# Performance work log

Measured on AMD Instinct MI355X. Metric: run time of the kernel, lower is better.

The kernel has to match this reference:

```python
import jax, jax.numpy as jnp
import numpy as np

B, D, ND, N2, H = 16384, 512, 4, 32, 4
C = D  # attention channels (per-detector feature dim)
EPS = 1e-5


def setup_inputs() -> dict:
    key = jax.random.key(0)
    ks = jax.random.split(key, 8)
    rn = lambda k, s, sc: jax.random.normal(k, s, jnp.float32) * sc
    return {
        'x': jax.random.normal(ks[0], (B, D), jnp.float32),
        'bn1_g': jnp.ones(D * ND, jnp.float32), 'bn1_b': jnp.zeros(D * ND, jnp.float32),
        'w1': rn(ks[1], (ND, D, D), 1e-4),  # diagonal blocks of the masked EnsembleLinear weight
        'bn2_g': jnp.ones(D * ND, jnp.float32), 'bn2_b': jnp.zeros(D * ND, jnp.float32),
        'wq': rn(ks[2], (C, D), 0.02), 'bq': jnp.zeros(C, jnp.float32),
        'wk': rn(ks[3], (C, D), 0.02), 'bk': jnp.zeros(C, jnp.float32),
        'wv': rn(ks[4], (C, D), 0.02), 'bv': jnp.zeros(C, jnp.float32),
        'wo': rn(ks[5], (C, C), 0.02), 'bo': jnp.zeros(C, jnp.float32),
        'ln1_g': jnp.ones(C, jnp.float32), 'ln1_b': jnp.zeros(C, jnp.float32),
        'wff': rn(ks[6], (C, C), 0.02), 'bff': jnp.zeros(C, jnp.float32),
        'ln2_g': jnp.ones(C, jnp.float32), 'ln2_b': jnp.zeros(C, jnp.float32),
        'w2': rn(ks[7], (ND, N2, D), 1e-4),
        'bn3_g': jnp.ones(N2 * ND, jnp.float32), 'bn3_b': jnp.zeros(N2 * ND, jnp.float32),
    }


def _batchnorm(x, g, b):
    # training-mode BatchNorm1d: biased batch stats over the batch axis
    m = x.mean(0)
    v = ((x - m) ** 2).mean(0)
    return (x - m) * jax.lax.rsqrt(v + EPS) * g + b


def _layernorm(x, g, b):
    m = x.mean(-1, keepdims=True)
    v = ((x - m) ** 2).mean(-1, keepdims=True)
    return (x - m) * jax.lax.rsqrt(v + EPS) * g + b


def reference(x, bn1_g, bn1_b, w1, bn2_g, bn2_b, wq, bq, wk, bk, wv, bv, wo, bo,
              ln1_g, ln1_b, wff, bff, ln2_g, ln2_b, w2, bn3_g, bn3_b):
    n = x.shape[0]
    # concat x num_detectors times along features: [n, ND*D]
    xc = jnp.tile(x, (1, ND))
    h = _batchnorm(xc, bn1_g, bn1_b)
    # EnsembleLinear 1: block-diagonal masked matmul == one small GEMM per detector
    h = jnp.einsum('ndi,doi->ndo', h.reshape(n, ND, D), w1).reshape(n, ND * D)
    h = jax.nn.sigmoid(_batchnorm(h, bn2_g, bn2_b))
    # 4-token self-attention over detectors: t is [n, ND, D]
    t = h.reshape(n, ND, D)
    hd = C // H
    q = (t @ wq.T + bq).reshape(n, ND, H, hd).transpose(0, 2, 1, 3)  # [n,H,S,hd]
    k = (t @ wk.T + bk).reshape(n, ND, H, hd).transpose(0, 2, 1, 3)
    v = (t @ wv.T + bv).reshape(n, ND, H, hd).transpose(0, 2, 1, 3)
    scale = jnp.sqrt(jnp.float32(C / H))
    scores = jnp.einsum('nhqd,nhkd->nhqk', q, k) / scale
    attn = jax.nn.softmax(scores, axis=-1)
    o = jnp.einsum('nhqk,nhkd->nhqd', attn, v).transpose(0, 2, 1, 3).reshape(n, ND, C)
    o = o @ wo.T + bo
    a1 = _layernorm(o + t, ln1_g, ln1_b)
    a2 = _layernorm(a1 @ wff.T + bff + a1, ln2_g, ln2_b)
    # EnsembleLinear 2: per-detector D -> N2
    h2 = jnp.einsum('ndi,doi->ndo', a2, w2).reshape(n, ND * N2)
    out = jax.nn.sigmoid(_batchnorm(h2, bn3_g, bn3_b))
    return out
```

## Files before the change

### kernel.cpp

```cpp
#include <hip/hip_runtime.h>
#include <hip/hip_bf16.h>

#define EPS 1e-5f

typedef __attribute__((ext_vector_type(8))) short bf16x8;
typedef __attribute__((ext_vector_type(4))) float f32x4;
typedef __attribute__((ext_vector_type(4))) float float4v;

__device__ __forceinline__ float b2f(short u) {
    union { unsigned int i; float f; } x;
    x.i = ((unsigned int)(unsigned short)u) << 16;
    return x.f;
}
__device__ __forceinline__ short f2b(float f) {
    unsigned int x = __builtin_bit_cast(unsigned int, f);
    unsigned int r = (x + 0x7FFFu + ((x >> 16) & 1u)) >> 16;
    return (short)r;
}

__device__ __forceinline__ void load_lds16(const void* g, void* l) {
    __builtin_amdgcn_global_load_lds(
        (const __attribute__((address_space(1))) unsigned int*)g,
        (__attribute__((address_space(3))) unsigned int*)l, 16, 0, 0);
}


__device__ __forceinline__ void cast8(const float* __restrict__ src, short* __restrict__ dst, long idx) {
    const float4v* s = (const float4v*)src;
    float4v a = s[idx * 2], b = s[idx * 2 + 1];
    bf16x8 o;
    o[0] = f2b(a[0]); o[1] = f2b(a[1]); o[2] = f2b(a[2]); o[3] = f2b(a[3]);
    o[4] = f2b(b[0]); o[5] = f2b(b[1]); o[6] = f2b(b[2]); o[7] = f2b(b[3]);
    *(bf16x8*)(dst + idx * 8) = o;
}

__global__ __launch_bounds__(256) void k_prep(
    const float* __restrict__ wq, const float* __restrict__ wk, const float* __restrict__ wv,
    const float* __restrict__ wo, const float* __restrict__ wff, const float* __restrict__ w2,
    const float* __restrict__ bq, const float* __restrict__ bk, const float* __restrict__ bv,
    short* __restrict__ Wqkvb, short* __restrict__ wo_b, short* __restrict__ wff_b,
    short* __restrict__ w2_b, float* __restrict__ bqkv) {
    int bid = blockIdx.x, tid = threadIdx.x;
    if (bid < 640) {
        int seg = bid >> 7;
        long idx = (long)(bid & 127) * 256 + tid;
        const float* src;
        short* dst;
        if (seg == 0) { src = wq; dst = Wqkvb; }
        else if (seg == 1) { src = wk; dst = Wqkvb + 262144; }
        else if (seg == 2) { src = wv; dst = Wqkvb + 524288; }
        else if (seg == 3) { src = wo; dst = wo_b; }
        else { src = wff; dst = wff_b; }
        cast8(src, dst, idx);
    } else if (bid < 672) {
        long idx = (long)(bid - 640) * 256 + tid;
        cast8(w2, w2_b, idx);
    } else {
        int i = (bid - 672) * 256 + tid;
        if (i < 512) bqkv[i] = bq[i];
        else if (i < 1024) bqkv[i] = bk[i - 512];
        else if (i < 1536) bqkv[i] = bv[i - 1024];
    }
}

__global__ __launch_bounds__(256) void k_statcast_x(const float* __restrict__ x,
                                                    short* __restrict__ xb,
                                                    float* __restrict__ psum, float* __restrict__ psq) {
    int b = blockIdx.x, tid = threadIdx.x;
    const float* xp = x + (long)b * 64 * 512;
    short* xo = xb + (long)b * 64 * 512;
    float s0 = 0, q0 = 0, s1 = 0, q1 = 0;
    for (int r = 0; r < 64; ++r) {
        float v0 = xp[r * 512 + tid];
        float v1 = xp[r * 512 + tid + 256];
        xo[r * 512 + tid] = f2b(v0);
        xo[r * 512 + tid + 256] = f2b(v1);
        s0 += v0; q0 += v0 * v0; s1 += v1; q1 += v1 * v1;
    }
    psum[b * 512 + tid] = s0; psum[b * 512 + tid + 256] = s1;
    psq[b * 512 + tid] = q0;  psq[b * 512 + tid + 256] = q1;
}


__global__ __launch_bounds__(256) void k_finalize_meanrs(const float* __restrict__ psum,
                                                         const float* __restrict__ psq,
                                                         int nparts, int ncols, float invB,
                                                         float* __restrict__ mean, float* __restrict__ rs) {
    int l = threadIdx.x & 63, grp = threadIdx.x >> 6;
    int c = blockIdx.x * 64 + l;
    float s = 0, q = 0;
    for (int p = grp; p < nparts; p += 4) {
        s += psum[(long)p * ncols + c];
        q += psq[(long)p * ncols + c];
    }
    __shared__ float rs_[4][64], rq_[4][64];
    rs_[grp][l] = s; rq_[grp][l] = q;
    __syncthreads();
    if (grp == 0) {
        s = rs_[0][l] + rs_[1][l] + rs_[2][l] + rs_[3][l];
        q = rq_[0][l] + rq_[1][l] + rq_[2][l] + rq_[3][l];
        float m = s * invB;
        float v = q * invB - m * m;
        mean[c] = m;
        rs[c] = rsqrtf(v + EPS);
    }
}

__global__ __launch_bounds__(256) void k_finalize_ss(const float* __restrict__ psum,
                                                     const float* __restrict__ psq,
                                                     int nparts, int ncols, float invB,
                                                     const float* __restrict__ g, const float* __restrict__ bb,
                                                     float* __restrict__ scale, float* __restrict__ shift) {
    int l = threadIdx.x & 63, grp = threadIdx.x >> 6;
    int c = blockIdx.x * 64 + l;
    float s = 0, q = 0;
    for (int p = grp; p < nparts; p += 4) {
        s += psum[(long)p * ncols + c];
        q += psq[(long)p * ncols + c];
    }
    __shared__ float rs_[4][64], rq_[4][64];
    rs_[grp][l] = s; rq_[grp][l] = q;
    __syncthreads();
    if (grp == 0) {
        s = rs_[0][l] + rs_[1][l] + rs_[2][l] + rs_[3][l];
        q = rq_[0][l] + rq_[1][l] + rq_[2][l] + rq_[3][l];
        float m = s * invB, v = q * invB - m * m;
        float sc = g[c] * rsqrtf(v + EPS);
        scale[c] = sc;
        shift[c] = bb[c] - m * sc;
    }
}

__global__ __launch_bounds__(256) void k_fold_w1(const float* __restrict__ w1, const float* __restrict__ g1,
                                                 const float* __restrict__ b1, const float* __restrict__ mean,
                                                 const float* __restrict__ rs,
                                                 short* __restrict__ W1b, float* __restrict__ beff) {
    int bx = blockIdx.x;
    int d = bx >> 9, tid = threadIdx.x;
    const float* wrow = w1 + (long)bx * 512;
    float part = 0.f;
    for (int i = tid; i < 512; i += 256) {
        float wv = wrow[i];
        float sc = rs[i] * g1[d * 512 + i];
        W1b[(long)bx * 512 + i] = f2b(wv * sc);
        part += (b1[d * 512 + i] - mean[i] * sc) * wv;
    }
    __shared__ float red[256];
    red[tid] = part;
    __syncthreads();
    for (int st = 128; st > 0; st >>= 1) {
        if (tid < st) red[tid] += red[tid + st];
        __syncthreads();
    }
    if (tid == 0) beff[bx] = red[0];
}

__global__ __launch_bounds__(256) void k_bnsig(const short* h, short* t,
                                               const float* __restrict__ scale,
                                               const float* __restrict__ shift) {
    long i8 = ((long)blockIdx.x * 256 + threadIdx.x) * 8;
    int c0 = (int)(i8 & 2047);
    bf16x8 v = *(const bf16x8*)(h + i8);
    bf16x8 o;
#pragma unroll
    for (int j = 0; j < 8; ++j) {
        float x = b2f(v[j]) * scale[c0 + j] + shift[c0 + j];
        o[j] = f2b(1.f / (1.f + __expf(-x)));
    }
    *(bf16x8*)(t + i8) = o;
}

__global__ __launch_bounds__(256) void k_ln(const short* in, short* out,
                                            const float* __restrict__ g, const float* __restrict__ bb) {
    int w = threadIdx.x >> 6, lane = threadIdx.x & 63;
    long row = (long)blockIdx.x * 4 + w;
    const short* rp = in + row * 512;
    bf16x8 v = *(const bf16x8*)(rp + lane * 8);
    float f[8];
    float s = 0.f;
#pragma unroll
    for (int j = 0; j < 8; ++j) { f[j] = b2f(v[j]); s += f[j]; }
#pragma unroll
    for (int m = 1; m < 64; m <<= 1) s += __shfl_xor(s, m, 64);
    float mean = s * (1.f / 512.f);
    float q = 0.f;
#pragma unroll
    for (int j = 0; j < 8; ++j) { float d = f[j] - mean; q += d * d; }
#pragma unroll
    for (int m = 1; m < 64; m <<= 1) q += __shfl_xor(q, m, 64);
    float rs = rsqrtf(q * (1.f / 512.f) + EPS);
    bf16x8 o;
#pragma unroll
    for (int j = 0; j < 8; ++j) {
        int c = lane * 8 + j;
        o[j] = f2b((f[j] - mean) * rs * g[c] + bb[c]);
    }
    *(bf16x8*)(out + row * 512 + lane * 8) = o;
}

__global__ __launch_bounds__(256) void k_bn3sig(const float* __restrict__ pre, float* __restrict__ out,
                                                const float* __restrict__ scale, const float* __restrict__ shift) {
    long i4 = ((long)blockIdx.x * 256 + threadIdx.x) * 4;
    float4v v = *(const float4v*)(pre + i4);
    int c0 = (int)(i4 & 127);
    float4v o;
#pragma unroll
    for (int j = 0; j < 4; ++j) {
        float x = v[j] * scale[c0 + j] + shift[c0 + j];
        o[j] = 1.f / (1.f + __expf(-x));
    }
    *(float4v*)(out + i4) = o;
}


template <int BM, int BN, int WGM, int WGN, bool ADD_RES, bool OUT_BF16>
__global__ __launch_bounds__(WGM* WGN * 64) void k_gemm_bt(
    const short* __restrict__ A, int a_zoff, int lda,
    const short* __restrict__ W, int w_zoff,
    const float* __restrict__ bias, int bias_zoff,
    short* Cb, float* Cf, int c_zoff, int ldc,
    const short* R, int ldr, int K) {
    constexpr int BK = 32;
    constexpr int WM = BM / WGM, WN = BN / WGN;
    constexpr int AM = WM / 16, AN = WN / 16;
    constexpr int NT = WGM * WGN * 64;
    constexpr int CH = (BM + BN) * (BK / 8);
    constexpr bool DBUF = (CH % NT == 0) && (CH / NT == 4);

    int tid = threadIdx.x;
    int wave = tid >> 6, lane = tid & 63;
    int wm = (wave % WGM) * WM, wn = (wave / WGM) * WN;

    int bm_idx = blockIdx.x, bn_idx = blockIdx.y;
    if (gridDim.z == 1 && (gridDim.x & 7) == 0) {
        int flat = blockIdx.x + gridDim.x * blockIdx.y;
        int k = flat & 7, l = flat >> 3;
        int j = l / gridDim.y;
        bn_idx = l - j * gridDim.y;
        bm_idx = k + 8 * j;
    }
    long m0 = (long)bm_idx * BM;
    int n0 = bn_idx * BN;
    int z = blockIdx.z;
    const short* Az = A + (long)z * a_zoff;
    const short* Wz = W + (long)z * w_zoff;

    f32x4 acc[AM][AN];
#pragma unroll
    for (int i = 0; i < AM; ++i)
#pragma unroll
        for (int j = 0; j < AN; ++j)
#pragma unroll
            for (int q = 0; q < 4; ++q) acc[i][j][q] = 0.f;

    int fr = lane & 15, ko = (lane >> 4) * 8;
    int cr = (lane >> 4) * 4, cc = lane & 15;

    if constexpr (DBUF) {
        __shared__ alignas(16) short Smem[2][(BM + BN) * BK];
        auto stage = [&](int b, int k0) {
#pragma unroll
            for (int i = 0; i < 4; ++i) {
                int c = tid + i * NT;
                int row = c >> 2, koff = (c & 3) * 8;
                const short* g = (row < BM) ? (Az + (m0 + row) * lda + k0 + koff)
                                            : (Wz + (long)(n0 + row - BM) * K + k0 + koff);
                load_lds16(g, (char*)Smem[b] + (size_t)c * 16);
            }
        };
        stage(0, 0);
        int nk = K / BK;
        for (int kt = 0; kt < nk; ++kt) {
            int b = kt & 1;
            if (kt + 1 < nk) {
                stage(b ^ 1, (kt + 1) * BK);
                asm volatile("s_waitcnt vmcnt(4)" ::: "memory");
            } else {
                asm volatile("s_waitcnt vmcnt(0)" ::: "memory");
            }
            __builtin_amdgcn_s_barrier();
            bf16x8 af[AM], bfr[AN];
#pragma unroll
            for (int i = 0; i < AM; ++i)
                af[i] = *(const bf16x8*)(&Smem[b][(wm + i * 16 + fr) * BK + ko]);
#pragma unroll
            for (int j = 0; j < AN; ++j)
                bfr[j] = *(const bf16x8*)(&Smem[b][(BM + wn + j * 16 + fr) * BK + ko]);
#pragma unroll
            for (int i = 0; i < AM; ++i)
#pragma unroll
                for (int j = 0; j < AN; ++j)
                    acc[i][j] = __builtin_amdgcn_mfma_f32_16x16x32_bf16(af[i], bfr[j], acc[i][j], 0, 0, 0);
            asm volatile("s_waitcnt lgkmcnt(0)" ::: "memory");
            __builtin_amdgcn_s_barrier();
        }
    } else {
        __shared__ alignas(16) short Smem[(BM + BN) * BK];
        for (int k0 = 0; k0 < K; k0 += BK) {
#pragma unroll
            for (int c = tid; c < CH; c += NT) {
                int row = c >> 2, koff = (c & 3) * 8;
                const short* g = (row < BM) ? (Az + (m0 + row) * lda + k0 + koff)
                                            : (Wz + (long)(n0 + row - BM) * K + k0 + koff);
                load_lds16(g, (char*)Smem + (size_t)c * 16);
            }
            __syncthreads();
            bf16x8 af[AM], bfr[AN];
#pragma unroll
            for (int i = 0; i < AM; ++i) af[i] = *(const bf16x8*)(&Smem[(wm + i * 16 + fr) * BK + ko]);
#pragma unroll
            for (int j = 0; j < AN; ++j) bfr[j] = *(const bf16x8*)(&Smem[(BM + wn + j * 16 + fr) * BK + ko]);
#pragma unroll
            for (int i = 0; i < AM; ++i)
#pragma unroll
                for (int j = 0; j < AN; ++j)
                    acc[i][j] = __builtin_amdgcn_mfma_f32_16x16x32_bf16(af[i], bfr[j], acc[i][j], 0, 0, 0);
            __syncthreads();
        }
    }

#pragma unroll
    for (int i = 0; i < AM; ++i) {
#pragma unroll
        for (int j = 0; j < AN; ++j) {
            int col = n0 + wn + j * 16 + cc;
            float bv = bias ? bias[(long)z * bias_zoff + col] : 0.f;
#pragma unroll
            for (int q = 0; q < 4; ++q) {
                long row = m0 + wm + i * 16 + cr + q;
                float v = acc[i][j][q] + bv;
                if constexpr (ADD_RES) v += b2f(R[row * (long)ldr + col]);
                long idx = row * (long)ldc + (long)z * c_zoff + col;
                if constexpr (OUT_BF16) Cb[idx] = f2b(v);
                else Cf[idx] = v;
            }
        }
    }
}


__global__ __launch_bounds__(256) void k_gemm_e1(
    const short* __restrict__ A, const short* __restrict__ W1, const float* __restrict__ beff,
    short* __restrict__ h, float* __restrict__ psum, float* __restrict__ psq) {
    constexpr int BK = 32;
    __shared__ alignas(16) short Smem[2][256 * BK];
    __shared__ float cS[2][128], cQ[2][128];

    int tid = threadIdx.x;
    int wave = tid >> 6, lane = tid & 63;
    int wm = (wave & 1) * 64, wn = (wave >> 1) * 64;
    long m0 = (long)blockIdx.x * 128;
    int n0 = blockIdx.y * 128;
    int z = blockIdx.z;
    const short* Wz = W1 + (long)z * 512 * 512;

    f32x4 acc[4][4];
#pragma unroll
    for (int i = 0; i < 4; ++i)
#pragma unroll
        for (int j = 0; j < 4; ++j)
#pragma unroll
            for (int q = 0; q < 4; ++q) acc[i][j][q] = 0.f;

    int fr = lane & 15, ko = (lane >> 4) * 8;

    auto stage = [&](int b, int k0) {
#pragma unroll
        for (int i = 0; i < 4; ++i) {
            int c = tid + i * 256;
            int row = c >> 2, koff = (c & 3) * 8;
            const short* g = (row < 128) ? (A + (m0 + row) * 512 + k0 + koff)
                                         : (Wz + (long)(n0 + row - 128) * 512 + k0 + koff);
            load_lds16(g, (char*)Smem[b] + (size_t)c * 16);
        }
    };
    stage(0, 0);
    for (int kt = 0; kt < 16; ++kt) {
        int b = kt & 1;
        if (kt + 1 < 16) {
            stage(b ^ 1, (kt + 1) * BK);
            asm volatile("s_waitcnt vmcnt(4)" ::: "memory");
        } else {
            asm volatile("s_waitcnt vmcnt(0)" ::: "memory");
        }
        __builtin_amdgcn_s_barrier();
        bf16x8 af[4], bfr[4];
#pragma unroll
        for (int i = 0; i < 4; ++i) af[i] = *(const bf16x8*)(&Smem[b][(wm + i * 16 + fr) * BK + ko]);
#pragma unroll
        for (int j = 0; j < 4; ++j) bfr[j] = *(const bf16x8*)(&Smem[b][(128 + wn + j * 16 + fr) * BK + ko]);
#pragma unroll
        for (int i = 0; i < 4; ++i)
#pragma unroll
            for (int j = 0; j < 4; ++j)
                acc[i][j] = __builtin_amdgcn_mfma_f32_16x16x32_bf16(af[i], bfr[j], acc[i][j], 0, 0, 0);
        asm volatile("s_waitcnt lgkmcnt(0)" ::: "memory");
        __builtin_amdgcn_s_barrier();
    }

    int cr = (lane >> 4) * 4, cc = lane & 15;
    float bv[4], colS[4], colQ[4];
#pragma unroll
    for (int j = 0; j < 4; ++j) {
        bv[j] = beff[z * 512 + n0 + wn + j * 16 + cc];
        colS[j] = 0.f; colQ[j] = 0.f;
    }
#pragma unroll
    for (int i = 0; i < 4; ++i)
#pragma unroll
        for (int j = 0; j < 4; ++j)
#pragma unroll
            for (int q = 0; q < 4; ++q) {
                float v = acc[i][j][q] + bv[j];
                acc[i][j][q] = v;
                colS[j] += v; colQ[j] += v * v;
            }
#pragma unroll
    for (int i = 0; i < 4; ++i)
#pragma unroll
        for (int q = 0; q < 4; ++q) {
            long row = m0 + wm + i * 16 + cr + q;
            short* hp = h + row * 2048 + z * 512 + n0 + wn + cc;
#pragma unroll
            for (int j = 0; j < 4; ++j) hp[j * 16] = f2b(acc[i][j][q]);
        }
#pragma unroll
    for (int j = 0; j < 4; ++j) {
        float s = colS[j], qq = colQ[j];
        s += __shfl_xor(s, 16, 64); s += __shfl_xor(s, 32, 64);
        qq += __shfl_xor(qq, 16, 64); qq += __shfl_xor(qq, 32, 64);
        if (lane < 16) { cS[wave & 1][wn + j * 16 + cc] = s; cQ[wave & 1][wn + j * 16 + cc] = qq; }
    }
    __syncthreads();
    if (tid < 128) {
        float S = cS[0][tid] + cS[1][tid];
        float Q = cQ[0][tid] + cQ[1][tid];
        psum[(long)blockIdx.x * 2048 + z * 512 + n0 + tid] = S;
        psq[(long)blockIdx.x * 2048 + z * 512 + n0 + tid] = Q;
    }
}


__global__ __launch_bounds__(256) void k_gemm_e2(
    const short* __restrict__ A, int a_zoff, int lda,
    const short* __restrict__ W2,
    float* __restrict__ Cf, int ldc,
    float* __restrict__ psum, float* __restrict__ psq) {
    constexpr int BK = 32;
    __shared__ alignas(16) short Smem[(128 + 32) * BK];
    __shared__ float cS[4][32], cQ[4][32];

    int tid = threadIdx.x;
    int wave = tid >> 6, lane = tid & 63;
    int wm = wave * 32;
    long m0 = (long)blockIdx.x * 128;
    int z = blockIdx.z;
    const short* Az = A + (long)z * a_zoff;
    const short* Wz = W2 + (long)z * 32 * 512;

    f32x4 acc[2][2];
#pragma unroll
    for (int i = 0; i < 2; ++i)
#pragma unroll
        for (int j = 0; j < 2; ++j)
#pragma unroll
            for (int q = 0; q < 4; ++q) acc[i][j][q] = 0.f;

    int fr = lane & 15, ko = (lane >> 4) * 8;

    for (int k0 = 0; k0 < 512; k0 += BK) {
        for (int c = tid; c < 640; c += 256) {
            int row = c >> 2, koff = (c & 3) * 8;
            const short* g = (row < 128) ? (Az + (m0 + row) * lda + k0 + koff)
                                         : (Wz + (long)(row - 128) * 512 + k0 + koff);
            load_lds16(g, (char*)Smem + (size_t)c * 16);
        }
        __syncthreads();
        bf16x8 af[2], bfr[2];
#pragma unroll
        for (int i = 0; i < 2; ++i) af[i] = *(const bf16x8*)(&Smem[(wm + i * 16 + fr) * BK + ko]);
#pragma unroll
        for (int j = 0; j < 2; ++j) bfr[j] = *(const bf16x8*)(&Smem[(128 + j * 16 + fr) * BK + ko]);
#pragma unroll
        for (int i = 0; i < 2; ++i)
#pragma unroll
            for (int j = 0; j < 2; ++j)
                acc[i][j] = __builtin_amdgcn_mfma_f32_16x16x32_bf16(af[i], bfr[j], acc[i][j], 0, 0, 0);
        __syncthreads();
    }

    int cr = (lane >> 4) * 4, cc = lane & 15;
    float colS[2] = {0.f, 0.f}, colQ[2] = {0.f, 0.f};
#pragma unroll
    for (int i = 0; i < 2; ++i)
#pragma unroll
        for (int q = 0; q < 4; ++q) {
            long row = m0 + wm + i * 16 + cr + q;
            float* cp = Cf + row * (long)ldc + z * 32 + cc;
#pragma unroll
            for (int j = 0; j < 2; ++j) {
                float v = acc[i][j][q];
                cp[j * 16] = v;
                colS[j] += v; colQ[j] += v * v;
            }
        }
#pragma unroll
    for (int j = 0; j < 2; ++j) {
        float s = colS[j], qq = colQ[j];
        s += __shfl_xor(s, 16, 64); s += __shfl_xor(s, 32, 64);
        qq += __shfl_xor(qq, 16, 64); qq += __shfl_xor(qq, 32, 64);
        if (lane < 16) { cS[wave][j * 16 + cc] = s; cQ[wave][j * 16 + cc] = qq; }
    }
    __syncthreads();
    if (tid < 32) {
        float S = cS[0][tid] + cS[1][tid] + cS[2][tid] + cS[3][tid];
        float Q = cQ[0][tid] + cQ[1][tid] + cQ[2][tid] + cQ[3][tid];
        psum[(long)blockIdx.x * 128 + z * 32 + tid] = S;
        psq[(long)blockIdx.x * 128 + z * 32 + tid] = Q;
    }
}

__global__ __launch_bounds__(256) void k_attn(const short* __restrict__ qkv, short* __restrict__ ao) {
    __shared__ alignas(16) short lds[4][4][1544];
    __shared__ float attn_s[4][4][4][4];
    int w = threadIdx.x >> 6, lane = threadIdx.x & 63;
    long n = (long)blockIdx.x * 4 + w;
    const short* src = qkv + n * 4 * 1536;
#pragma unroll
    for (int c = 0; c < 12; ++c) {
        int e = c * 512 + lane * 8;
        *(bf16x8*)(&lds[w][e / 1536][e % 1536]) = *(const bf16x8*)(src + e);
    }
    __syncthreads();
    int h = lane >> 4, a = (lane >> 2) & 3, b = lane & 3;
    const short* qp = &lds[w][a][h * 128];
    const short* kp = &lds[w][b][512 + h * 128];
    float s = 0.f;
#pragma unroll
    for (int j = 0; j < 128; j += 8) {
        bf16x8 qv = *(const bf16x8*)(qp + j);
        bf16x8 kv = *(const bf16x8*)(kp + j);
#pragma unroll
        for (int x = 0; x < 8; ++x) s += b2f(qv[x]) * b2f(kv[x]);
    }
    s *= 0.08838834764831845f;
    float mx = fmaxf(s, __shfl_xor(s, 1, 64));
    mx = fmaxf(mx, __shfl_xor(mx, 2, 64));
    float e = __expf(s - mx);
    float den = e + __shfl_xor(e, 1, 64);
    den += __shfl_xor(den, 2, 64);
    attn_s[w][h][a][b] = e / den;
    __syncthreads();
    int ta = lane >> 4, cg = lane & 15;
#pragma unroll
    for (int hh = 0; hh < 4; ++hh) {
        int c0 = hh * 128 + cg * 8;
        float at0 = attn_s[w][hh][ta][0], at1 = attn_s[w][hh][ta][1];
        float at2 = attn_s[w][hh][ta][2], at3 = attn_s[w][hh][ta][3];
        bf16x8 v0 = *(const bf16x8*)(&lds[w][0][1024 + c0]);
        bf16x8 v1 = *(const bf16x8*)(&lds[w][1][1024 + c0]);
        bf16x8 v2 = *(const bf16x8*)(&lds[w][2][1024 + c0]);
        bf16x8 v3 = *(const bf16x8*)(&lds[w][3][1024 + c0]);
        bf16x8 ov;
#pragma unroll
        for (int j = 0; j < 8; ++j) {
            float val = at0 * b2f(v0[j]) + at1 * b2f(v1[j]) + at2 * b2f(v2[j]) + at3 * b2f(v3[j]);
            ov[j] = f2b(val);
        }
        *(bf16x8*)(ao + (n * 4 + ta) * 512 + c0) = ov;
    }
}


extern "C" void kernel_launch(void* const* d_in, const int* in_sizes, int n_in,
                              void* d_out, int out_size, void* d_ws, size_t ws_size,
                              hipStream_t stream) {
    const float* x = (const float*)d_in[0];
    const float* bn1_g = (const float*)d_in[1];
    const float* bn1_b = (const float*)d_in[2];
    const float* w1 = (const float*)d_in[3];
    const float* bn2_g = (const float*)d_in[4];
    const float* bn2_b = (const float*)d_in[5];
    const float* wq = (const float*)d_in[6];
    const float* bq = (const float*)d_in[7];
    const float* wk = (const float*)d_in[8];
    const float* bk = (const float*)d_in[9];
    const float* wv = (const float*)d_in[10];
    const float* bv = (const float*)d_in[11];
    const float* wo = (const float*)d_in[12];
    const float* bo = (const float*)d_in[13];
    const float* ln1_g = (const float*)d_in[14];
    const float* ln1_b = (const float*)d_in[15];
    const float* wff = (const float*)d_in[16];
    const float* bff = (const float*)d_in[17];
    const float* ln2_g = (const float*)d_in[18];
    const float* ln2_b = (const float*)d_in[19];
    const float* w2 = (const float*)d_in[20];
    const float* bn3_g = (const float*)d_in[21];
    const float* bn3_b = (const float*)d_in[22];
    float* out = (float*)d_out;

    char* ws = (char*)d_ws;
    size_t off = 0;
    auto alloc = [&](size_t bytes) {
        void* p = ws + off;
        off = (off + bytes + 255) & ~(size_t)255;
        return p;
    };

    short* W1b = (short*)alloc(4l * 512 * 512 * 2);
    float* beff = (float*)alloc(4l * 512 * 4);
    short* Wqkvb = (short*)alloc(1536l * 512 * 2);
    float* bqkv = (float*)alloc(1536l * 4);
    short* wo_b = (short*)alloc(512l * 512 * 2);
    short* wff_b = (short*)alloc(512l * 512 * 2);
    short* w2_b = (short*)alloc(4l * 32 * 512 * 2);
    float* mean1 = (float*)alloc(512 * 4);
    float* rs1 = (float*)alloc(512 * 4);
    float* scale2 = (float*)alloc(2048 * 4);
    float* shift2 = (float*)alloc(2048 * 4);
    float* scale3 = (float*)alloc(128 * 4);
    float* shift3 = (float*)alloc(128 * 4);
    float* psum1 = (float*)alloc(256l * 512 * 4);
    float* psq1 = (float*)alloc(256l * 512 * 4);
    float* psum2 = (float*)alloc(128l * 2048 * 4);
    float* psq2 = (float*)alloc(128l * 2048 * 4);
    float* psum3 = (float*)alloc(256l * 128 * 4);
    float* psq3 = (float*)alloc(256l * 128 * 4);
    short* slotA = (short*)alloc(16384l * 2048 * 2);
    float* out_pre = (float*)alloc(16384l * 128 * 4);
    short* bufB = (short*)alloc(16384l * 2048 * 2);

    long NCq = 1024;
    for (long cand = 16384; cand >= 1024; cand >>= 1) {
        if (off + (size_t)cand * 12288 + (1u << 20) <= ws_size) { NCq = cand; break; }
    }
    short* qkv_c = (short*)alloc((size_t)NCq * 12288);
    short* xb = bufB;

    dim3 B256(256);

    hipLaunchKernelGGL(k_prep, dim3(678), B256, 0, stream,
                       wq, wk, wv, wo, wff, w2, bq, bk, bv,
                       Wqkvb, wo_b, wff_b, w2_b, bqkv);
    hipLaunchKernelGGL(k_statcast_x, dim3(256), B256, 0, stream, x, xb, psum1, psq1);

    hipLaunchKernelGGL(k_finalize_meanrs, dim3(8), B256, 0, stream, psum1, psq1, 256, 512,
                       1.f / 16384.f, mean1, rs1);
    hipLaunchKernelGGL(k_fold_w1, dim3(2048), B256, 0, stream, w1, bn1_g, bn1_b, mean1, rs1, W1b, beff);

    hipLaunchKernelGGL(k_gemm_e1, dim3(128, 4, 4), B256, 0, stream,
                       xb, W1b, beff, slotA, psum2, psq2);

    hipLaunchKernelGGL(k_finalize_ss, dim3(32), B256, 0, stream, psum2, psq2, 128, 2048,
                       1.f / 16384.f, bn2_g, bn2_b, scale2, shift2);
    hipLaunchKernelGGL(k_bnsig, dim3(16384), B256, 0, stream, slotA, slotA, scale2, shift2);

    long nch = 16384 / NCq;
    for (long c = 0; c < nch; ++c) {
        long r0 = c * NCq;
        const short* t_c = slotA + r0 * 2048;
        int gx = (int)(NCq * 4 / 128);

        hipLaunchKernelGGL((k_gemm_bt<128, 128, 2, 2, false, true>), dim3(gx, 12, 1), B256, 0, stream,
                           t_c, 0, 512, Wqkvb, 0, bqkv, 0,
                           qkv_c, (float*)nullptr, 0, 1536, (const short*)nullptr, 0, 512);

        hipLaunchKernelGGL(k_attn, dim3((int)(NCq / 4)), B256, 0, stream,
                           qkv_c, bufB + r0 * 2048);
    }

    hipLaunchKernelGGL((k_gemm_bt<128, 128, 2, 2, true, true>), dim3(512, 4, 1), B256, 0, stream,
                       bufB, 0, 512, wo_b, 0, bo, 0,
                       slotA, (float*)nullptr, 0, 512, slotA, 512, 512);

    hipLaunchKernelGGL(k_ln, dim3(16384), B256, 0, stream, slotA, slotA, ln1_g, ln1_b);

    hipLaunchKernelGGL((k_gemm_bt<128, 128, 2, 2, true, true>), dim3(512, 4, 1), B256, 0, stream,
                       slotA, 0, 512, wff_b, 0, bff, 0,
                       bufB, (float*)nullptr, 0, 512, slotA, 512, 512);

    hipLaunchKernelGGL(k_ln, dim3(16384), B256, 0, stream, bufB, bufB, ln2_g, ln2_b);

    hipLaunchKernelGGL(k_gemm_e2, dim3(128, 1, 4), B256, 0, stream,
                       bufB, 512, 2048, w2_b, out_pre, 128, psum3, psq3);

    hipLaunchKernelGGL(k_finalize_ss, dim3(2), B256, 0, stream, psum3, psq3, 128, 128,
                       1.f / 16384.f, bn3_g, bn3_b, scale3, shift3);
    hipLaunchKernelGGL(k_bn3sig, dim3(2048), B256, 0, stream, out_pre, out, scale3, shift3);
}
```

Before: 553.0 us.

## Fuse output/FFN GEMMs with residual add and LayerNorm into one kernel

Adds a GEMM kernel whose 64-row block tile spans all 512 output columns. This lets it add bias and residual, reduce row mean and variance across its 8 waves through shared memory, and write the LayerNorm result directly. It replaces the two GEMM plus separate LayerNorm pairs, removing two full read/write passes over the 65536x512 bf16 activation and two launches. In exchange the GEMM mainloop is single-buffered and every block re-reads the whole 512x512 weight, which should come from L2. Variance is now computed as E[x^2]-mean^2, which is slightly less numerically robust.

New measurement: 587.9 us. +6.3%, slower.

```diff
diff --git a/kernel.cpp b/kernel.cpp
--- a/kernel.cpp
+++ b/kernel.cpp
@@ -170,34 +170,6 @@
     *(bf16x8*)(t + i8) = o;
 }
 
-__global__ __launch_bounds__(256) void k_ln(const short* in, short* out,
-                                            const float* __restrict__ g, const float* __restrict__ bb) {
-    int w = threadIdx.x >> 6, lane = threadIdx.x & 63;
-    long row = (long)blockIdx.x * 4 + w;
-    const short* rp = in + row * 512;
-    bf16x8 v = *(const bf16x8*)(rp + lane * 8);
-    float f[8];
-    float s = 0.f;
-#pragma unroll
-    for (int j = 0; j < 8; ++j) { f[j] = b2f(v[j]); s += f[j]; }
-#pragma unroll
-    for (int m = 1; m < 64; m <<= 1) s += __shfl_xor(s, m, 64);
-    float mean = s * (1.f / 512.f);
-    float q = 0.f;
-#pragma unroll
-    for (int j = 0; j < 8; ++j) { float d = f[j] - mean; q += d * d; }
-#pragma unroll
-    for (int m = 1; m < 64; m <<= 1) q += __shfl_xor(q, m, 64);
-    float rs = rsqrtf(q * (1.f / 512.f) + EPS);
-    bf16x8 o;
-#pragma unroll
-    for (int j = 0; j < 8; ++j) {
-        int c = lane * 8 + j;
-        o[j] = f2b((f[j] - mean) * rs * g[c] + bb[c]);
-    }
-    *(bf16x8*)(out + row * 512 + lane * 8) = o;
-}
-
 __global__ __launch_bounds__(256) void k_bn3sig(const float* __restrict__ pre, float* __restrict__ out,
                                                 const float* __restrict__ scale, const float* __restrict__ shift) {
     long i4 = ((long)blockIdx.x * 256 + threadIdx.x) * 4;
@@ -334,6 +306,98 @@
                 if constexpr (OUT_BF16) Cb[idx] = f2b(v);
                 else Cf[idx] = v;
             }
+        }
+    }
+}
+
+
+__global__ __launch_bounds__(512) void k_gemm_lnf(
+    const short* __restrict__ A, const short* __restrict__ W,
+    const float* __restrict__ bias, const short* R,
+    const float* __restrict__ g, const float* __restrict__ bb,
+    short* C) {
+    constexpr int BK = 32;
+    __shared__ alignas(16) short Smem[(64 + 512) * BK];
+    __shared__ float rS[64][8], rQ[64][8];
+
+    int tid = threadIdx.x, wave = tid >> 6, lane = tid & 63;
+    int wn = wave * 64;
+    long m0 = (long)blockIdx.x * 64;
+    int fr = lane & 15, hi = lane >> 4, ko = hi * 8;
+
+    f32x4 acc[4][4];
+#pragma unroll
+    for (int i = 0; i < 4; ++i)
+#pragma unroll
+        for (int j = 0; j < 4; ++j)
+#pragma unroll
+            for (int q = 0; q < 4; ++q) acc[i][j][q] = 0.f;
+
+    for (int k0 = 0; k0 < 512; k0 += BK) {
+        for (int c = tid; c < 2304; c += 512) {
+            int row = c >> 2, koff = (c & 3) * 8;
+            const short* gp = (row < 64) ? (A + (m0 + row) * 512 + k0 + koff)
+                                         : (W + (long)(row - 64) * 512 + k0 + koff);
+            load_lds16(gp, (char*)Smem + (size_t)c * 16);
+        }
+        __syncthreads();
+        bf16x8 af[4], bfr[4];
+#pragma unroll
+        for (int i = 0; i < 4; ++i) af[i] = *(const bf16x8*)(&Smem[(i * 16 + fr) * BK + ko]);
+#pragma unroll
+        for (int j = 0; j < 4; ++j) bfr[j] = *(const bf16x8*)(&Smem[(64 + wn + j * 16 + fr) * BK + ko]);
+#pragma unroll
+        for (int i = 0; i < 4; ++i)
+#pragma unroll
+            for (int j = 0; j < 4; ++j)
+                acc[i][j] = __builtin_amdgcn_mfma_f32_16x16x32_bf16(af[i], bfr[j], acc[i][j], 0, 0, 0);
+        __syncthreads();
+    }
+
+    int cr = hi * 4, cc = fr;
+    float bj[4], gj[4], bbj[4];
+#pragma unroll
+    for (int j = 0; j < 4; ++j) {
+        int col = wn + j * 16 + cc;
+        bj[j] = bias[col]; gj[j] = g[col]; bbj[j] = bb[col];
+    }
+
+#pragma unroll
+    for (int i = 0; i < 4; ++i) {
+#pragma unroll
+        for (int q = 0; q < 4; ++q) {
+            int rl = i * 16 + cr + q;
+            const short* rp = R + (m0 + rl) * 512 + wn + cc;
+            float s = 0.f, qq = 0.f;
+#pragma unroll
+            for (int j = 0; j < 4; ++j) {
+                float v = acc[i][j][q] + bj[j] + b2f(rp[j * 16]);
+                acc[i][j][q] = v;
+                s += v; qq += v * v;
+            }
+            s += __shfl_xor(s, 1, 64); qq += __shfl_xor(qq, 1, 64);
+            s += __shfl_xor(s, 2, 64); qq += __shfl_xor(qq, 2, 64);
+            s += __shfl_xor(s, 4, 64); qq += __shfl_xor(qq, 4, 64);
+            s += __shfl_xor(s, 8, 64); qq += __shfl_xor(qq, 8, 64);
+            if (cc == 0) { rS[rl][wave] = s; rQ[rl][wave] = qq; }
+        }
+    }
+    __syncthreads();
+#pragma unroll
+    for (int i = 0; i < 4; ++i) {
+#pragma unroll
+        for (int q = 0; q < 4; ++q) {
+            int rl = i * 16 + cr + q;
+            float S = rS[rl][0] + rS[rl][1] + rS[rl][2] + rS[rl][3]
+                    + rS[rl][4] + rS[rl][5] + rS[rl][6] + rS[rl][7];
+            float Q = rQ[rl][0] + rQ[rl][1] + rQ[rl][2] + rQ[rl][3]
+                    + rQ[rl][4] + rQ[rl][5] + rQ[rl][6] + rQ[rl][7];
+            float mean = S * (1.f / 512.f);
+            float rstd = rsqrtf(Q * (1.f / 512.f) - mean * mean + EPS);
+            short* cp = C + (m0 + rl) * 512 + wn + cc;
+#pragma unroll
+            for (int j = 0; j < 4; ++j)
+                cp[j * 16] = f2b((acc[i][j][q] - mean) * rstd * gj[j] + bbj[j]);
         }
     }
 }
@@ -670,17 +734,11 @@
                            qkv_c, bufB + r0 * 2048);
     }
 
-    hipLaunchKernelGGL((k_gemm_bt<128, 128, 2, 2, true, true>), dim3(512, 4, 1), B256, 0, stream,
-                       bufB, 0, 512, wo_b, 0, bo, 0,
-                       slotA, (float*)nullptr, 0, 512, slotA, 512, 512);
-
-    hipLaunchKernelGGL(k_ln, dim3(16384), B256, 0, stream, slotA, slotA, ln1_g, ln1_b);
-
-    hipLaunchKernelGGL((k_gemm_bt<128, 128, 2, 2, true, true>), dim3(512, 4, 1), B256, 0, stream,
-                       slotA, 0, 512, wff_b, 0, bff, 0,
-                       bufB, (float*)nullptr, 0, 512, slotA, 512, 512);
-
-    hipLaunchKernelGGL(k_ln, dim3(16384), B256, 0, stream, bufB, bufB, ln2_g, ln2_b);
+    hipLaunchKernelGGL(k_gemm_lnf, dim3(1024), dim3(512), 0, stream,
+                       bufB, wo_b, bo, slotA, ln1_g, ln1_b, slotA);
+
+    hipLaunchKernelGGL(k_gemm_lnf, dim3(1024), dim3(512), 0, stream,
+                       slotA, wff_b, bff, slotA, ln2_g, ln2_b, bufB);
 
     hipLaunchKernelGGL(k_gemm_e2, dim3(128, 1, 4), B256, 0, stream,
                        bufB, 512, 2048, w2_b, out_pre, 128, psum3, psq3);
```
